# Optimization experiments

Measured on AMD Instinct MI355X. Metric: run time of the kernel, lower is better.

The kernel has to match this reference:

```python
import jax, jax.numpy as jnp
import numpy as np


def _rotate_matrices(angles):
    # angles: (M, 1) -> rot (M, 2, 2), rows [[c, -s], [s, c]]
    c = jnp.cos(angles)
    s = jnp.sin(angles)
    rot = jnp.stack([jnp.concatenate([c, -s], axis=1),
                     jnp.concatenate([s, c], axis=1)], axis=1)
    return rot, jnp.swapaxes(rot, 1, 2)


def _seq_group_permute(x, mapping, perms, final=False):
    # x: (B, S, d), perms: (d//2, 2, 2)
    B, S, d = x.shape
    if not final:
        x = x[:, :, mapping]
    x = x.reshape(B, S, d // 2, 2)
    x = jnp.einsum('ijmk,mkn->ijmn', x, perms).reshape(B, S, d)
    if final:
        x = x[:, :, mapping]
    return x


def _mat_group_permute_inv(m, mapping, perms_inv, transposed):
    # m: (R, d), perms_inv: (d//2, 2, 2)
    R, d = m.shape
    m = m[:, mapping].reshape(R, d // 2, 2)
    sub = 'imk,mkn->imn' if transposed else 'imk,mnk->imn'
    return jnp.einsum(sub, m, perms_inv).reshape(R, d)


def setup_inputs() -> dict:
    key = jax.random.key(0)
    ks = jax.random.split(key, 8)
    B, S, IN, OUT = 4, 2048, 1024, 4096
    inp = jax.random.normal(ks[0], (B, S, IN), dtype=jnp.float32)
    weight = jax.random.normal(ks[1], (OUT, IN), dtype=jnp.float32) * 0.02
    mask = (jax.random.uniform(ks[2], (OUT, IN)) > 0.5).astype(jnp.float32)
    in_scores = jax.random.normal(ks[3], (IN // 2, 1), dtype=jnp.float32)
    out_scores = jax.random.normal(ks[4], (OUT // 2, 1), dtype=jnp.float32)
    in_mapping = jax.random.permutation(ks[5], IN).astype(jnp.int32)
    out_mapping = jax.random.permutation(ks[6], OUT).astype(jnp.int32)
    out_mapping_reverse = jnp.argsort(out_mapping).astype(jnp.int32)
    return {
        'input': inp,
        'weight': weight,
        'mask': mask,
        'in_permutation_scores': in_scores,
        'out_permutation_scores': out_scores,
        'in_mapping': in_mapping,
        'out_mapping': out_mapping,
        'out_mapping_reverse': out_mapping_reverse,
        'temperature': 1,
    }


def reference(input, weight, mask, in_permutation_scores, out_permutation_scores,
              in_mapping, out_mapping, out_mapping_reverse, temperature):
    in_permut, in_permut_inv = _rotate_matrices(in_permutation_scores)
    out_permut, out_permut_inv = _rotate_matrices(out_permutation_scores)
    # permute + rotate activations on the input side
    s_in = _seq_group_permute(input, in_mapping, in_permut)
    # inverse permute/rotate the weight's input dim, then its output dim
    m2 = _mat_group_permute_inv(weight, in_mapping, in_permut_inv, transposed=False)
    m3 = _mat_group_permute_inv(m2.T, out_mapping, out_permut_inv, transposed=True)
    m3 = m3 * mask.T  # (in, out)
    s_inner = jnp.einsum('bsi,io->bso', s_in, m3)
    s_out = _seq_group_permute(s_inner, out_mapping_reverse, out_permut, final=True)
    return s_out
```

## Files before the change

kernel.cpp:

```cpp
#include <hip/hip_runtime.h>
#include <hip/hip_bf16.h>
#include <stdint.h>

#define M_DIM 8192
#define K_DIM 1024
#define N_DIM 4096

typedef __bf16 bf16x8 __attribute__((ext_vector_type(8)));
typedef float  f32x4  __attribute__((ext_vector_type(4)));

__device__ __forceinline__ uint16_t f2bf(float f) {
  union { float f; uint32_t u; } x; x.f = f;
  uint32_t u = x.u;
  return (uint16_t)((u + 0x7FFFu + ((u >> 16) & 1u)) >> 16);
}

__global__ __launch_bounds__(256) void convert_bf16_kernel(
    const float* __restrict__ in, uint16_t* __restrict__ out, int n4) {
  int i = blockIdx.x * 256 + threadIdx.x;
  if (i >= n4) return;
  float4 v = ((const float4*)in)[i];
  ushort4 o;
  o.x = f2bf(v.x); o.y = f2bf(v.y); o.z = f2bf(v.z); o.w = f2bf(v.w);
  ((ushort4*)out)[i] = o;
}

__global__ __launch_bounds__(256) void build_w_kernel(
    const float* __restrict__ weight,
    const float* __restrict__ mask,
    const float* __restrict__ in_scores,
    const float* __restrict__ out_scores,
    const int*   __restrict__ in_mapping,
    const int*   __restrict__ out_mapping,
    uint16_t*    __restrict__ w5t)
{
  __shared__ float    w0[K_DIM], w1[K_DIM];
  __shared__ uint16_t o0[K_DIM], o1[K_DIM];

  const int mo = blockIdx.x;
  const int t  = threadIdx.x;

  const int r0 = out_mapping[2 * mo];
  const int r1 = out_mapping[2 * mo + 1];

  ((float4*)w0)[t] = ((const float4*)(weight + (size_t)r0 * K_DIM))[t];
  ((float4*)w1)[t] = ((const float4*)(weight + (size_t)r1 * K_DIM))[t];

  const float ao = out_scores[mo];
  const float so = sinf(ao), co = cosf(ao);

  __syncthreads();

#pragma unroll
  for (int s = 0; s < 2; s++) {
    const int mi = t + s * 256;
    const float ai = in_scores[mi];
    const float si = sinf(ai), ci = cosf(ai);
    const int ia0 = in_mapping[2 * mi];
    const int ia1 = in_mapping[2 * mi + 1];

    const float w00 = w0[ia0], w01 = w0[ia1];
    const float w10 = w1[ia0], w11 = w1[ia1];

    float a00 =  ci * w00 + si * w01;
    float a01 = -si * w00 + ci * w01;
    float a10 =  ci * w10 + si * w11;
    float a11 = -si * w10 + ci * w11;

    float b00 = co * a00 - so * a10;
    float b10 = co * a01 - so * a11;
    float b01 = so * a00 + co * a10;
    float b11 = so * a01 + co * a11;

    const float2 mk0 = *(const float2*)&mask[(size_t)(2 * mo) * K_DIM + 2 * mi];
    const float2 mk1 = *(const float2*)&mask[(size_t)(2 * mo + 1) * K_DIM + 2 * mi];
    b00 *= mk0.x; b10 *= mk0.y;
    b01 *= mk1.x; b11 *= mk1.y;

    float c00 =  co * b00 + so * b01;
    float c10 =  co * b10 + so * b11;
    float c01 = -so * b00 + co * b01;
    float c11 = -so * b10 + co * b11;

    o0[ia0] = f2bf(ci * c00 - si * c10);
    o0[ia1] = f2bf(si * c00 + ci * c10);
    o1[ia0] = f2bf(ci * c01 - si * c11);
    o1[ia1] = f2bf(si * c01 + ci * c11);
  }

  __syncthreads();

  ((uint2*)(w5t + (size_t)r0 * K_DIM))[t] = ((const uint2*)o0)[t];
  ((uint2*)(w5t + (size_t)r1 * K_DIM))[t] = ((const uint2*)o1)[t];
}


__device__ __forceinline__ void async_load16(const uint16_t* g, uint16_t* lds_wave_uniform) {
  __builtin_amdgcn_global_load_lds(
      (const __attribute__((address_space(1))) uint32_t*)g,
      (__attribute__((address_space(3))) uint32_t*)lds_wave_uniform,
      16, 0, 0);
}

__global__ __launch_bounds__(256, 2) void gemm_kernel(
    const uint16_t* __restrict__ A,
    const uint16_t* __restrict__ BT,
    float* __restrict__ C)
{
  __shared__ __align__(16) uint16_t As[128 * 32];
  __shared__ __align__(16) uint16_t Bs[128 * 32];

  const int tid  = threadIdx.x;
  const int wave = tid >> 6;
  const int lane = tid & 63;
  const int quad = lane >> 4;
  const int rr   = lane & 15;
  const int bn   = blockIdx.x;
  const int bm   = blockIdx.y;
  const int wm   = (wave >> 1) * 64;
  const int wn   = (wave & 1) * 64;

  f32x4 acc[4][4] = {};

  const int row0 = tid >> 2;
  const int kb   = (lane & 3) * 8;
  const uint16_t* gA0 = A  + (size_t)(bm * 128 + row0) * K_DIM + kb;
  const uint16_t* gA1 = A  + (size_t)(bm * 128 + row0 + 64) * K_DIM + kb;
  const uint16_t* gB0 = BT + (size_t)(bn * 128 + row0) * K_DIM + kb;
  const uint16_t* gB1 = BT + (size_t)(bn * 128 + row0 + 64) * K_DIM + kb;
  uint16_t* lA0 = &As[wave * 512];
  uint16_t* lA1 = &As[2048 + wave * 512];
  uint16_t* lB0 = &Bs[wave * 512];
  uint16_t* lB1 = &Bs[2048 + wave * 512];

  for (int k0 = 0; k0 < K_DIM; k0 += 32) {
    async_load16(gA0 + k0, lA0);
    async_load16(gA1 + k0, lA1);
    async_load16(gB0 + k0, lB0);
    async_load16(gB1 + k0, lB1);
    __syncthreads();

    bf16x8 af[4], bfr[4];
#pragma unroll
    for (int i = 0; i < 4; i++)
      af[i] = *reinterpret_cast<const bf16x8*>(&As[(wm + i * 16 + rr) * 32 + quad * 8]);
#pragma unroll
    for (int j = 0; j < 4; j++)
      bfr[j] = *reinterpret_cast<const bf16x8*>(&Bs[(wn + j * 16 + rr) * 32 + quad * 8]);

#pragma unroll
    for (int i = 0; i < 4; i++)
#pragma unroll
      for (int j = 0; j < 4; j++)
        acc[i][j] = __builtin_amdgcn_mfma_f32_16x16x32_bf16(af[i], bfr[j], acc[i][j], 0, 0, 0);

    __syncthreads();
  }

#pragma unroll
  for (int i = 0; i < 4; i++) {
#pragma unroll
    for (int j = 0; j < 4; j++) {
      const int colg = bn * 128 + wn + j * 16 + rr;
#pragma unroll
      for (int rg = 0; rg < 4; rg++) {
        const int rowg = bm * 128 + wm + i * 16 + quad * 4 + rg;
        C[(size_t)rowg * N_DIM + colg] = acc[i][j][rg];
      }
    }
  }
}

extern "C" void kernel_launch(void* const* d_in, const int* in_sizes, int n_in,
                              void* d_out, int out_size, void* d_ws, size_t ws_size,
                              hipStream_t stream) {
  const float* input      = (const float*)d_in[0];
  const float* weight     = (const float*)d_in[1];
  const float* mask       = (const float*)d_in[2];
  const float* in_scores  = (const float*)d_in[3];
  const float* out_scores = (const float*)d_in[4];
  const int*   in_mapping = (const int*)d_in[5];
  const int*   out_mapping= (const int*)d_in[6];
  float* out = (float*)d_out;

  uint16_t* a_bf16 = (uint16_t*)d_ws;
  uint16_t* w5t    = (uint16_t*)d_ws + (size_t)M_DIM * K_DIM;

  convert_bf16_kernel<<<(M_DIM * K_DIM / 4 + 255) / 256, 256, 0, stream>>>(
      input, a_bf16, M_DIM * K_DIM / 4);

  build_w_kernel<<<2048, 256, 0, stream>>>(
      weight, mask, in_scores, out_scores, in_mapping, out_mapping, w5t);

  dim3 grid(N_DIM / 128, M_DIM / 128);
  gemm_kernel<<<grid, 256, 0, stream>>>(a_bf16, w5t, out);
}
```

Baseline: 264.3 us.

## Double GEMM K-tile to 64 and XOR-swizzle LDS layout

Widens the per-iteration K slice of the bf16 GEMM from 32 to 64, halving the number of loop iterations and barrier pairs. It also stores each 16-byte chunk of A and B tiles in LDS at an XOR-swizzled position, using the row index, to avoid bank conflicts on the fragment reads. The cost is double the LDS per block (32 KB), which may limit occupancy, and still no double buffering of global loads.

```diff
diff --git a/kernel.cpp b/kernel.cpp
--- a/kernel.cpp
+++ b/kernel.cpp
@@ -107,8 +107,8 @@
     const uint16_t* __restrict__ BT,
     float* __restrict__ C)
 {
-  __shared__ __align__(16) uint16_t As[128 * 32];
-  __shared__ __align__(16) uint16_t Bs[128 * 32];
+  __shared__ __align__(16) uint16_t As[128 * 64];
+  __shared__ __align__(16) uint16_t Bs[128 * 64];
 
   const int tid  = threadIdx.x;
   const int wave = tid >> 6;
@@ -122,37 +122,57 @@
 
   f32x4 acc[4][4] = {};
 
-  const int row0 = tid >> 2;
-  const int kb   = (lane & 3) * 8;
-  const uint16_t* gA0 = A  + (size_t)(bm * 128 + row0) * K_DIM + kb;
-  const uint16_t* gA1 = A  + (size_t)(bm * 128 + row0 + 64) * K_DIM + kb;
-  const uint16_t* gB0 = BT + (size_t)(bn * 128 + row0) * K_DIM + kb;
-  const uint16_t* gB1 = BT + (size_t)(bn * 128 + row0 + 64) * K_DIM + kb;
-  uint16_t* lA0 = &As[wave * 512];
-  uint16_t* lA1 = &As[2048 + wave * 512];
-  uint16_t* lB0 = &Bs[wave * 512];
-  uint16_t* lB1 = &Bs[2048 + wave * 512];
-
-  for (int k0 = 0; k0 < K_DIM; k0 += 32) {
-    async_load16(gA0 + k0, lA0);
-    async_load16(gA1 + k0, lA1);
-    async_load16(gB0 + k0, lB0);
-    async_load16(gB1 + k0, lB1);
+  const uint16_t* gA[4];
+  const uint16_t* gB[4];
+  uint16_t* lA[4];
+  uint16_t* lB[4];
+#pragma unroll
+  for (int it = 0; it < 4; it++) {
+    const int c   = it * 256 + tid;
+    const int row = c >> 3;
+    const int h   = c & 7;
+    const int g   = h ^ (row & 7);
+    gA[it] = A  + (size_t)(bm * 128 + row) * K_DIM + g * 8;
+    gB[it] = BT + (size_t)(bn * 128 + row) * K_DIM + g * 8;
+    lA[it] = &As[(it * 256 + wave * 64) * 8];
+    lB[it] = &Bs[(it * 256 + wave * 64) * 8];
+  }
+
+  for (int k0 = 0; k0 < K_DIM; k0 += 64) {
+#pragma unroll
+    for (int it = 0; it < 4; it++) {
+      async_load16(gA[it] + k0, lA[it]);
+      async_load16(gB[it] + k0, lB[it]);
+    }
     __syncthreads();
 
-    bf16x8 af[4], bfr[4];
-#pragma unroll
-    for (int i = 0; i < 4; i++)
-      af[i] = *reinterpret_cast<const bf16x8*>(&As[(wm + i * 16 + rr) * 32 + quad * 8]);
-#pragma unroll
-    for (int j = 0; j < 4; j++)
-      bfr[j] = *reinterpret_cast<const bf16x8*>(&Bs[(wn + j * 16 + rr) * 32 + quad * 8]);
-
-#pragma unroll
-    for (int i = 0; i < 4; i++)
-#pragma unroll
-      for (int j = 0; j < 4; j++)
-        acc[i][j] = __builtin_amdgcn_mfma_f32_16x16x32_bf16(af[i], bfr[j], acc[i][j], 0, 0, 0);
+    bf16x8 af[4][2], bfr[4][2];
+#pragma unroll
+    for (int i = 0; i < 4; i++) {
+      const int r = wm + i * 16 + rr;
+#pragma unroll
+      for (int s = 0; s < 2; s++) {
+        const int gk = s * 4 + quad;
+        af[i][s] = *reinterpret_cast<const bf16x8*>(&As[(r * 8 + (gk ^ (r & 7))) * 8]);
+      }
+    }
+#pragma unroll
+    for (int j = 0; j < 4; j++) {
+      const int r = wn + j * 16 + rr;
+#pragma unroll
+      for (int s = 0; s < 2; s++) {
+        const int gk = s * 4 + quad;
+        bfr[j][s] = *reinterpret_cast<const bf16x8*>(&Bs[(r * 8 + (gk ^ (r & 7))) * 8]);
+      }
+    }
+
+#pragma unroll
+    for (int s = 0; s < 2; s++)
+#pragma unroll
+      for (int i = 0; i < 4; i++)
+#pragma unroll
+        for (int j = 0; j < 4; j++)
+          acc[i][j] = __builtin_amdgcn_mfma_f32_16x16x32_bf16(af[i][s], bfr[j][s], acc[i][j], 0, 0, 0);
 
     __syncthreads();
   }
```

Measured after the change: 259.1 us. -2.0%, faster.
